# Kernel tuning notes

Hardware: AMD Instinct MI355X
Metric: run time of the kernel (lower is better)

Reference implementation:

```python
import jax, jax.numpy as jnp
import numpy as np

LN_EPS = 1e-5
NORM_EPS = 1e-12


def channel_layernorm(x, w, b):
    # LayerNorm over channel dim of NCHW tensor (torch permutes to NHWC; equivalent)
    mu = x.mean(axis=1, keepdims=True)
    var = x.var(axis=1, keepdims=True)
    xn = (x - mu) / jnp.sqrt(var + LN_EPS)
    return xn * w[None, :, None, None] + b[None, :, None, None]


def pconv(x, w):
    # 1x1 pointwise conv, w: (out_ch, in_ch)
    return jnp.einsum('bchw,oc->bohw', x, w)


def dwconv3(x, w):
    # depthwise 3x3, padding 1; w: (ch, 1, 3, 3)
    return jax.lax.conv_general_dilated(
        x, w, window_strides=(1, 1), padding='SAME',
        feature_group_count=x.shape[1],
        dimension_numbers=('NCHW', 'OIHW', 'NCHW'))


def l2norm(x):
    n = jnp.sqrt(jnp.sum(x * x, axis=-1, keepdims=True))
    return x / jnp.maximum(n, NORM_EPS)


def setup_inputs() -> dict:
    key = jax.random.key(0)
    ks = jax.random.split(key, 8)
    B, C, H, W = 4, 128, 128, 128
    NH, G = 8, 2

    def w(k, shape, fan_in):
        return jax.random.normal(k, shape, dtype=jnp.float32) * (fan_in ** -0.5)

    return {
        'x': jax.random.normal(ks[0], (B, C, H, W), dtype=jnp.float32),
        'ln1_w': jnp.ones((C,), jnp.float32),
        'ln1_b': jnp.zeros((C,), jnp.float32),
        'temperature': jnp.ones((NH, 1, 1), jnp.float32),
        'qkv_p_w': w(ks[1], (3 * C, C), C),
        'qkv_d_w': w(ks[2], (3 * C, 1, 3, 3), 9),
        'proj_w': w(ks[3], (C, C), C),
        'ln2_w': jnp.ones((C,), jnp.float32),
        'ln2_b': jnp.zeros((C,), jnp.float32),
        'g1_w': w(ks[4], (2 * G * C, C), C),
        'gd_w': w(ks[5], (2 * G * C, 1, 3, 3), 9),
        'g2_w': w(ks[6], (C, G * C), G * C),
        'num_heads': NH,
    }


def reference(x, ln1_w, ln1_b, temperature, qkv_p_w, qkv_d_w, proj_w,
              ln2_w, ln2_b, g1_w, gd_w, g2_w, num_heads):
    b, c, h, w_ = x.shape
    d = c // num_heads

    # --- MDTA branch ---
    y = channel_layernorm(x, ln1_w, ln1_b)
    qkv = dwconv3(pconv(y, qkv_p_w), qkv_d_w)  # (b, 3c, h, w)
    q, k, v = jnp.split(qkv, 3, axis=1)
    q = l2norm(q.reshape(b, num_heads, d, h * w_))
    k = l2norm(k.reshape(b, num_heads, d, h * w_))
    v = v.reshape(b, num_heads, d, h * w_)
    # transposed (channel) attention: (b, heads, d, d)
    attn = jnp.einsum('bhdn,bhen->bhde', q, k) * temperature[None]
    attn = jax.nn.softmax(attn, axis=-1)
    out = jnp.einsum('bhde,bhen->bhdn', attn, v).reshape(b, c, h, w_)
    x = x + pconv(out, proj_w)

    # --- GDFN branch ---
    y = channel_layernorm(x, ln2_w, ln2_b)
    hdn = dwconv3(pconv(y, g1_w), gd_w)  # (b, 2*gamma*c, h, w)
    x1, x2 = jnp.split(hdn, 2, axis=1)
    g = jax.nn.gelu(x1, approximate=False) * x2
    x = x + pconv(g, g2_w)
    return x
```

## Files before the change

### kernel.cpp

```cpp
#include <hip/hip_runtime.h>
#include <cstdint>
#include <cstddef>

typedef float f32x4 __attribute__((ext_vector_type(4)));
typedef __bf16 bf16x8 __attribute__((ext_vector_type(8)));

__device__ __forceinline__ float b2f(unsigned short u) {
    union { unsigned int i; float f; } z; z.i = ((unsigned int)u) << 16; return z.f;
}
__device__ __forceinline__ unsigned short f2b(float f) {
    union { float f; unsigned int i; } z; z.f = f;
    unsigned int x = z.i;
    return (unsigned short)((x + 0x7FFFu + ((x >> 16) & 1u)) >> 16);
}

static constexpr int C = 128;
static constexpr int NP = 16384;
static constexpr int NH = 8;

struct Ptr11 { const float* p[11]; };
__constant__ int kWN[11]   = {128, 128, 8, 49152, 3456, 16384, 128, 128, 65536, 4608, 32768};
__constant__ int kWOff[11] = {0, 128, 256, 272, 49424, 52880, 69264, 69392, 69520, 135056, 139664};
static constexpr int kWTotal = 172432;

__global__ __launch_bounds__(256)
void cvt_w_kernel(Ptr11 P, unsigned short* __restrict__ dst)
{
    int seg = blockIdx.y;
    int n = kWN[seg];
    int i = blockIdx.x * 256 + threadIdx.x;
    if (i >= n) return;
    dst[kWOff[seg] + i] = f2b(P.p[seg][i]);
}

template <int COUT>
__device__ __forceinline__ void gemm_core_128(
    const unsigned short (*Bs)[128],
    const unsigned short* __restrict__ W,
    unsigned short* __restrict__ OutB,
    int n0, int tid)
{
    const int lane = tid & 63;
    const int wid  = tid >> 6;
    const int ln16 = lane & 15, quad = lane >> 4;
    const int wy = wid >> 1, wx = wid & 1;
    for (int cc = 0; cc < COUT / 128; ++cc) {
        const int m0 = cc * 128;
        f32x4 acc[4][4];
        #pragma unroll
        for (int i = 0; i < 4; ++i)
            #pragma unroll
            for (int j = 0; j < 4; ++j) acc[i][j] = f32x4{0.f, 0.f, 0.f, 0.f};

        #pragma unroll
        for (int k0 = 0; k0 < 128; k0 += 32) {
            bf16x8 afr[4], bfr[4];
            #pragma unroll
            for (int mt = 0; mt < 4; ++mt) {
                int m = m0 + wy * 64 + mt * 16 + ln16;
                uint4 v = *(const uint4*)(W + (size_t)m * 128 + k0 + quad * 8);
                afr[mt] = *(bf16x8*)&v;
            }
            #pragma unroll
            for (int nt = 0; nt < 4; ++nt) {
                int n = wx * 64 + nt * 16 + ln16;
                union { bf16x8 v; unsigned short u[8]; } tmp;
                #pragma unroll
                for (int j = 0; j < 8; ++j) tmp.u[j] = Bs[k0 + quad * 8 + j][n];
                bfr[nt] = tmp.v;
            }
            #pragma unroll
            for (int mt = 0; mt < 4; ++mt)
                #pragma unroll
                for (int nt = 0; nt < 4; ++nt)
                    acc[mt][nt] = __builtin_amdgcn_mfma_f32_16x16x32_bf16(
                        afr[mt], bfr[nt], acc[mt][nt], 0, 0, 0);
        }
        #pragma unroll
        for (int mt = 0; mt < 4; ++mt)
            #pragma unroll
            for (int nt = 0; nt < 4; ++nt) {
                int co0 = m0 + wy * 64 + mt * 16 + quad * 4;
                int n = n0 + wx * 64 + nt * 16 + ln16;
                #pragma unroll
                for (int r = 0; r < 4; ++r)
                    OutB[(size_t)(co0 + r) * NP + n] = f2b(acc[mt][nt][r]);
            }
    }
}

template <int COUT>
__global__ __launch_bounds__(256)
void lngemm_kernel(const float* __restrict__ x,
                   const unsigned short* __restrict__ lg,
                   const unsigned short* __restrict__ lb,
                   const unsigned short* __restrict__ W,
                   unsigned short* __restrict__ Out)
{
    __shared__ unsigned short Bs[128][128];
    __shared__ float Ssum[8][128], Ssq[8][128], Mu[128], Rs[128];
    const int tid = threadIdx.x;
    const int b = blockIdx.y;
    const int n0 = blockIdx.x * 128;
    const int pxg = tid & 31;
    const int cseg = tid >> 5;
    const float* xb = x + (size_t)b * C * NP + n0 + pxg * 4;

    f32x4 hv[16];
    f32x4 vs = f32x4{0.f, 0.f, 0.f, 0.f}, vq = f32x4{0.f, 0.f, 0.f, 0.f};
    #pragma unroll
    for (int i = 0; i < 16; ++i) {
        f32x4 v = *(const f32x4*)(xb + (size_t)(cseg * 16 + i) * NP);
        hv[i] = v; vs += v; vq += v * v;
    }
    #pragma unroll
    for (int j = 0; j < 4; ++j) {
        Ssum[cseg][pxg * 4 + j] = vs[j];
        Ssq[cseg][pxg * 4 + j]  = vq[j];
    }
    __syncthreads();
    if (tid < 128) {
        float s = 0.f, q = 0.f;
        #pragma unroll
        for (int e = 0; e < 8; ++e) { s += Ssum[e][tid]; q += Ssq[e][tid]; }
        float mu = s * (1.f / 128.f);
        float var = q * (1.f / 128.f) - mu * mu;
        Mu[tid] = mu;
        Rs[tid] = rsqrtf(fmaxf(var, 0.f) + 1e-5f);
    }
    __syncthreads();
    f32x4 mu4 = *(const f32x4*)(&Mu[pxg * 4]);
    f32x4 rs4 = *(const f32x4*)(&Rs[pxg * 4]);
    #pragma unroll
    for (int i = 0; i < 16; ++i) {
        int c = cseg * 16 + i;
        float gw = b2f(lg[c]), bw = b2f(lb[c]);
        union { uint2 v; unsigned short u[4]; } o;
        #pragma unroll
        for (int j = 0; j < 4; ++j)
            o.u[j] = f2b((hv[i][j] - mu4[j]) * rs4[j] * gw + bw);
        *(uint2*)(&Bs[c][pxg * 4]) = o.v;
    }
    __syncthreads();
    gemm_core_128<COUT>(Bs, W, Out + (size_t)b * COUT * NP, n0, tid);
}

template <int COUT>
__global__ __launch_bounds__(256)
void gemm_bf16_kernel(const unsigned short* __restrict__ W,
                      const unsigned short* __restrict__ X,
                      unsigned short* __restrict__ Out)
{
    __shared__ unsigned short Bs[128][128];
    const int tid = threadIdx.x;
    const int b = blockIdx.y;
    const int n0 = blockIdx.x * 128;
    const unsigned short* Xb = X + (size_t)b * 128 * NP;
    #pragma unroll
    for (int r = 0; r < 8; ++r) {
        int flat = tid + r * 256;
        int kk = flat >> 4, nn = (flat & 15) * 8;
        *(uint4*)(&Bs[kk][nn]) = *(const uint4*)(Xb + (size_t)kk * NP + n0 + nn);
    }
    __syncthreads();
    gemm_core_128<COUT>(Bs, W, Out + (size_t)b * COUT * NP, n0, tid);
}

__global__ __launch_bounds__(256)
void projln_kernel(const unsigned short* __restrict__ W,
                   const unsigned short* __restrict__ Xin,
                   const float* __restrict__ Res,
                   float* __restrict__ Xmid,
                   const unsigned short* __restrict__ lg,
                   const unsigned short* __restrict__ lb,
                   unsigned short* __restrict__ Y2)
{
    __shared__ unsigned short Bs[128][128];
    __shared__ float RedS[2][128], RedQ[2][128], Mu[128], Rs[128];
    const int tid = threadIdx.x;
    const int b = blockIdx.y;
    const int n0 = blockIdx.x * 128;
    const unsigned short* Xb = Xin + (size_t)b * 128 * NP;
    #pragma unroll
    for (int r = 0; r < 8; ++r) {
        int flat = tid + r * 256;
        int kk = flat >> 4, nn = (flat & 15) * 8;
        *(uint4*)(&Bs[kk][nn]) = *(const uint4*)(Xb + (size_t)kk * NP + n0 + nn);
    }
    __syncthreads();

    const int lane = tid & 63, wid = tid >> 6;
    const int ln16 = lane & 15, quad = lane >> 4;
    const int wy = wid >> 1, wx = wid & 1;

    f32x4 acc[4][4];
    #pragma unroll
    for (int i = 0; i < 4; ++i)
        #pragma unroll
        for (int j = 0; j < 4; ++j) acc[i][j] = f32x4{0.f, 0.f, 0.f, 0.f};

    #pragma unroll
    for (int k0 = 0; k0 < 128; k0 += 32) {
        bf16x8 afr[4], bfr[4];
        #pragma unroll
        for (int mt = 0; mt < 4; ++mt) {
            int m = wy * 64 + mt * 16 + ln16;
            uint4 v = *(const uint4*)(W + (size_t)m * 128 + k0 + quad * 8);
            afr[mt] = *(bf16x8*)&v;
        }
        #pragma unroll
        for (int nt = 0; nt < 4; ++nt) {
            int n = wx * 64 + nt * 16 + ln16;
            union { bf16x8 v; unsigned short u[8]; } tmp;
            #pragma unroll
            for (int j = 0; j < 8; ++j) tmp.u[j] = Bs[k0 + quad * 8 + j][n];
            bfr[nt] = tmp.v;
        }
        #pragma unroll
        for (int mt = 0; mt < 4; ++mt)
            #pragma unroll
            for (int nt = 0; nt < 4; ++nt)
                acc[mt][nt] = __builtin_amdgcn_mfma_f32_16x16x32_bf16(
                    afr[mt], bfr[nt], acc[mt][nt], 0, 0, 0);
    }

    size_t base = (size_t)b * 128 * NP;
    float ps[4] = {0.f, 0.f, 0.f, 0.f}, pq[4] = {0.f, 0.f, 0.f, 0.f};
    #pragma unroll
    for (int mt = 0; mt < 4; ++mt)
        #pragma unroll
        for (int nt = 0; nt < 4; ++nt) {
            int co0 = wy * 64 + mt * 16 + quad * 4;
            int n = n0 + wx * 64 + nt * 16 + ln16;
            #pragma unroll
            for (int r = 0; r < 4; ++r) {
                size_t idx = base + (size_t)(co0 + r) * NP + n;
                float t = Res[idx] + acc[mt][nt][r];
                Xmid[idx] = t;
                acc[mt][nt][r] = t;
                ps[nt] += t; pq[nt] += t * t;
            }
        }
    #pragma unroll
    for (int nt = 0; nt < 4; ++nt) {
        ps[nt] += __shfl_xor(ps[nt], 16, 64); ps[nt] += __shfl_xor(ps[nt], 32, 64);
        pq[nt] += __shfl_xor(pq[nt], 16, 64); pq[nt] += __shfl_xor(pq[nt], 32, 64);
    }
    if (quad == 0) {
        #pragma unroll
        for (int nt = 0; nt < 4; ++nt) {
            int nn = wx * 64 + nt * 16 + ln16;
            RedS[wy][nn] = ps[nt]; RedQ[wy][nn] = pq[nt];
        }
    }
    __syncthreads();
    if (tid < 128) {
        float s = RedS[0][tid] + RedS[1][tid];
        float q = RedQ[0][tid] + RedQ[1][tid];
        float mu = s * (1.f / 128.f);
        float var = q * (1.f / 128.f) - mu * mu;
        Mu[tid] = mu; Rs[tid] = rsqrtf(fmaxf(var, 0.f) + 1e-5f);
    }
    __syncthreads();

    #pragma unroll
    for (int mt = 0; mt < 4; ++mt) {
        int co0 = wy * 64 + mt * 16 + quad * 4;
        union { uint2 v; unsigned short u[4]; } gv, bv;
        gv.v = *(const uint2*)(lg + co0);
        bv.v = *(const uint2*)(lb + co0);
        float gw[4], bw[4];
        #pragma unroll
        for (int r = 0; r < 4; ++r) { gw[r] = b2f(gv.u[r]); bw[r] = b2f(bv.u[r]); }
        #pragma unroll
        for (int nt = 0; nt < 4; ++nt) {
            int nn = wx * 64 + nt * 16 + ln16;
            float mu = Mu[nn], rs = Rs[nn];
            int n = n0 + nn;
            #pragma unroll
            for (int r = 0; r < 4; ++r) {
                size_t idx = base + (size_t)(co0 + r) * NP + n;
                Y2[idx] = f2b((acc[mt][nt][r] - mu) * rs * gw[r] + bw[r]);
            }
        }
    }
}

template <int K, int EPI>
__global__ __launch_bounds__(256)
void gemm_pconv(const unsigned short* __restrict__ W,
                const unsigned short* __restrict__ X,
                void* __restrict__ Out,
                const float* __restrict__ Res,
                int Cout)
{
    __shared__ unsigned short Bs[32][128];
    const int tid = threadIdx.x;
    const int b = blockIdx.z;
    const int n0 = blockIdx.x * 128;
    const int m0 = blockIdx.y * 128;
    const unsigned short* Xb = X + (size_t)b * K * NP;
    const int wid = tid >> 6;
    const int lane = tid & 63;
    const int ln16 = lane & 15;
    const int quad = lane >> 4;
    const int wy = wid >> 1;
    const int wx = wid & 1;

    f32x4 acc[4][4];
    #pragma unroll
    for (int i = 0; i < 4; ++i)
        #pragma unroll
        for (int j = 0; j < 4; ++j)
            acc[i][j] = f32x4{0.f, 0.f, 0.f, 0.f};

    for (int k0 = 0; k0 < K; k0 += 32) {
        #pragma unroll
        for (int r = 0; r < 2; ++r) {
            int flat = tid + r * 256;
            int kk = flat >> 4;
            int nn = (flat & 15) * 8;
            uint4 v = *(const uint4*)(Xb + (size_t)(k0 + kk) * NP + n0 + nn);
            *(uint4*)(&Bs[kk][nn]) = v;
        }
        __syncthreads();

        bf16x8 afr[4];
        #pragma unroll
        for (int mt = 0; mt < 4; ++mt) {
            int m = m0 + wy * 64 + mt * 16 + ln16;
            uint4 v = *(const uint4*)(W + (size_t)m * K + k0 + quad * 8);
            afr[mt] = *(bf16x8*)&v;
        }
        bf16x8 bfr[4];
        #pragma unroll
        for (int nt = 0; nt < 4; ++nt) {
            int n = wx * 64 + nt * 16 + ln16;
            union { bf16x8 v; unsigned short u[8]; } tmp;
            #pragma unroll
            for (int j = 0; j < 8; ++j) tmp.u[j] = Bs[quad * 8 + j][n];
            bfr[nt] = tmp.v;
        }
        #pragma unroll
        for (int mt = 0; mt < 4; ++mt)
            #pragma unroll
            for (int nt = 0; nt < 4; ++nt)
                acc[mt][nt] = __builtin_amdgcn_mfma_f32_16x16x32_bf16(
                    afr[mt], bfr[nt], acc[mt][nt], 0, 0, 0);
        __syncthreads();
    }

    size_t outbase = (size_t)b * Cout * NP;
    #pragma unroll
    for (int mt = 0; mt < 4; ++mt) {
        #pragma unroll
        for (int nt = 0; nt < 4; ++nt) {
            int co0 = m0 + wy * 64 + mt * 16 + quad * 4;
            int n = n0 + wx * 64 + nt * 16 + ln16;
            #pragma unroll
            for (int r = 0; r < 4; ++r) {
                float v = acc[mt][nt][r];
                size_t idx = outbase + (size_t)(co0 + r) * NP + n;
                if (EPI == 0) ((unsigned short*)Out)[idx] = f2b(v);
                else          ((float*)Out)[idx] = Res[idx] + v;
            }
        }
    }
}

__global__ __launch_bounds__(256)
void dwconv3_kernel(const unsigned short* __restrict__ in,
                    const unsigned short* __restrict__ w9,
                    unsigned short* __restrict__ out, int CH)
{
    int t = blockIdx.x * 256 + threadIdx.x;
    int xi = (t & 15) * 8;
    int y  = (t >> 4) & 127;
    int bc = t >> 11;
    int c  = bc % CH;
    const unsigned short* base = in + (size_t)bc * NP + y * 128 + xi;

    float wr[9];
    #pragma unroll
    for (int i = 0; i < 9; ++i) wr[i] = b2f(w9[c * 9 + i]);

    uint4 rv0 = uint4{0,0,0,0}, rv1, rv2 = uint4{0,0,0,0};
    if (y > 0)   rv0 = *(const uint4*)(base - 128);
    rv1 = *(const uint4*)(base);
    if (y < 127) rv2 = *(const uint4*)(base + 128);
    uint4 rows[3] = {rv0, rv1, rv2};

    float o[8];
    #pragma unroll
    for (int j = 0; j < 8; ++j) o[j] = 0.f;

    #pragma unroll
    for (int r = 0; r < 3; ++r) {
        union { uint4 v; unsigned short u[8]; } cv; cv.v = rows[r];
        int lh = __shfl_up((int)cv.u[7], 1, 16);
        int rh = __shfl_down((int)cv.u[0], 1, 16);
        float p[10];
        p[0] = (xi > 0)   ? b2f((unsigned short)lh) : 0.f;
        p[9] = (xi < 120) ? b2f((unsigned short)rh) : 0.f;
        #pragma unroll
        for (int j = 0; j < 8; ++j) p[j + 1] = b2f(cv.u[j]);
        #pragma unroll
        for (int j = 0; j < 8; ++j)
            o[j] += wr[r * 3] * p[j] + wr[r * 3 + 1] * p[j + 1] + wr[r * 3 + 2] * p[j + 2];
    }
    union { uint4 v; unsigned short u[8]; } res;
    #pragma unroll
    for (int j = 0; j < 8; ++j) res.u[j] = f2b(o[j]);
    *(uint4*)(out + (size_t)bc * NP + y * 128 + xi) = res.v;
}

__global__ __launch_bounds__(256)
void dwgelu_kernel(const unsigned short* __restrict__ hdn,
                   const unsigned short* __restrict__ w9,
                   unsigned short* __restrict__ g)
{
    int t = blockIdx.x * 256 + threadIdx.x;
    int xi = (t & 15) * 8;
    int y  = (t >> 4) & 127;
    int bc = t >> 11;
    int c  = bc & 255;
    int b  = bc >> 8;
    const unsigned short* base1 = hdn + ((size_t)b * 512 + c) * NP + y * 128 + xi;
    const unsigned short* base2 = base1 + (size_t)256 * NP;

    float w1[9], w2[9];
    #pragma unroll
    for (int i = 0; i < 9; ++i) {
        w1[i] = b2f(w9[c * 9 + i]);
        w2[i] = b2f(w9[(c + 256) * 9 + i]);
    }

    uint4 ra0 = uint4{0,0,0,0}, ra1, ra2 = uint4{0,0,0,0};
    uint4 rb0 = uint4{0,0,0,0}, rb1, rb2 = uint4{0,0,0,0};
    if (y > 0)   { ra0 = *(const uint4*)(base1 - 128); rb0 = *(const uint4*)(base2 - 128); }
    ra1 = *(const uint4*)(base1);
    rb1 = *(const uint4*)(base2);
    if (y < 127) { ra2 = *(const uint4*)(base1 + 128); rb2 = *(const uint4*)(base2 + 128); }
    uint4 rowsA[3] = {ra0, ra1, ra2};
    uint4 rowsB[3] = {rb0, rb1, rb2};

    float a1[8], a2[8];
    #pragma unroll
    for (int j = 0; j < 8; ++j) { a1[j] = 0.f; a2[j] = 0.f; }

    #pragma unroll
    for (int r = 0; r < 3; ++r) {
        union { uint4 v; unsigned short u[8]; } c1, c2;
        c1.v = rowsA[r]; c2.v = rowsB[r];
        int lh1 = __shfl_up((int)c1.u[7], 1, 16);
        int rh1 = __shfl_down((int)c1.u[0], 1, 16);
        int lh2 = __shfl_up((int)c2.u[7], 1, 16);
        int rh2 = __shfl_down((int)c2.u[0], 1, 16);
        float p1[10], p2[10];
        p1[0] = (xi > 0)   ? b2f((unsigned short)lh1) : 0.f;
        p1[9] = (xi < 120) ? b2f((unsigned short)rh1) : 0.f;
        p2[0] = (xi > 0)   ? b2f((unsigned short)lh2) : 0.f;
        p2[9] = (xi < 120) ? b2f((unsigned short)rh2) : 0.f;
        #pragma unroll
        for (int j = 0; j < 8; ++j) { p1[j + 1] = b2f(c1.u[j]); p2[j + 1] = b2f(c2.u[j]); }
        #pragma unroll
        for (int j = 0; j < 8; ++j) {
            a1[j] += w1[r * 3] * p1[j] + w1[r * 3 + 1] * p1[j + 1] + w1[r * 3 + 2] * p1[j + 2];
            a2[j] += w2[r * 3] * p2[j] + w2[r * 3 + 1] * p2[j + 1] + w2[r * 3 + 2] * p2[j + 2];
        }
    }
    union { uint4 v; unsigned short u[8]; } res;
    #pragma unroll
    for (int j = 0; j < 8; ++j) {
        float u = a1[j];
        float tt = u * (0.7978845608f + 0.0356774081f * u * u);
        float e = __expf(2.f * tt);
        float th = 1.f - 2.f / (e + 1.f);
        float ge = 0.5f * u * (1.f + th);
        res.u[j] = f2b(ge * a2[j]);
    }
    *(uint4*)(g + (size_t)bc * NP + y * 128 + xi) = res.v;
}

__global__ __launch_bounds__(256)
void gramss_kernel(const unsigned short* __restrict__ qkv,
                   float* __restrict__ Spart, float* __restrict__ Npart)
{
    int h = blockIdx.x, b = blockIdx.y, sp = blockIdx.z;
    int wid = threadIdx.x >> 6, lane = threadIdx.x & 63;
    int ln16 = lane & 15, quad = lane >> 4;
    int nbase = sp * 2048 + wid * 512;
    const unsigned short* qp = qkv + ((size_t)b * 384 + h * 16 + ln16) * NP;
    const unsigned short* kp = qkv + ((size_t)b * 384 + 128 + h * 16 + ln16) * NP;
    f32x4 acc = f32x4{0.f, 0.f, 0.f, 0.f};
    float qs = 0.f, ks = 0.f;
    for (int i = 0; i < 512; i += 32) {
        int n = nbase + i + quad * 8;
        uint4 av = *(const uint4*)(qp + n);
        uint4 bv = *(const uint4*)(kp + n);
        union { uint4 v; unsigned short u[8]; } ua, ub;
        ua.v = av; ub.v = bv;
        #pragma unroll
        for (int j = 0; j < 8; ++j) {
            float qv = b2f(ua.u[j]); qs += qv * qv;
            float kv = b2f(ub.u[j]); ks += kv * kv;
        }
        acc = __builtin_amdgcn_mfma_f32_16x16x32_bf16(*(bf16x8*)&av, *(bf16x8*)&bv, acc, 0, 0, 0);
    }
    int bh = b * NH + h;
    float* Sp = Spart + ((size_t)bh * 32 + sp * 4 + wid) * 256;
    #pragma unroll
    for (int r = 0; r < 4; ++r)
        Sp[(quad * 4 + r) * 16 + ln16] = acc[r];

    qs += __shfl_xor(qs, 16, 64); qs += __shfl_xor(qs, 32, 64);
    ks += __shfl_xor(ks, 16, 64); ks += __shfl_xor(ks, 32, 64);
    __shared__ float G[4][32];
    if (quad == 0) { G[wid][ln16] = qs; G[wid][16 + ln16] = ks; }
    __syncthreads();
    if (threadIdx.x < 32) {
        float s = G[0][threadIdx.x] + G[1][threadIdx.x] + G[2][threadIdx.x] + G[3][threadIdx.x];
        Npart[((size_t)bh * 8 + sp) * 32 + threadIdx.x] = s;
    }
}

__global__ __launch_bounds__(256)
void softmax2_kernel(const float* __restrict__ Spart, const float* __restrict__ Npart,
                     const unsigned short* __restrict__ temp, float* __restrict__ P)
{
    int bh = blockIdx.x;
    int h = bh & 7;
    int t = threadIdx.x;
    int dq = t >> 4, dk = t & 15;
    float sacc = 0.f;
    const float* Sp = Spart + (size_t)bh * 32 * 256;
    #pragma unroll
    for (int j = 0; j < 32; ++j) sacc += Sp[j * 256 + t];
    const float* Np = Npart + (size_t)bh * 8 * 32;
    float sq = 0.f, sk = 0.f;
    #pragma unroll
    for (int sp = 0; sp < 8; ++sp) { sq += Np[sp * 32 + dq]; sk += Np[sp * 32 + 16 + dk]; }
    float nq = fmaxf(sqrtf(sq), 1e-12f);
    float nk = fmaxf(sqrtf(sk), 1e-12f);
    float v = sacc / (nq * nk) * b2f(temp[h]);
    float m = v;
    #pragma unroll
    for (int o = 8; o > 0; o >>= 1) m = fmaxf(m, __shfl_xor(m, o, 16));
    float e = __expf(v - m);
    float s = e;
    #pragma unroll
    for (int o = 8; o > 0; o >>= 1) s += __shfl_xor(s, o, 16);
    P[(size_t)bh * 256 + t] = e / s;
}

__global__ __launch_bounds__(256)
void attnv_kernel(const float* __restrict__ P, const unsigned short* __restrict__ qkv,
                  unsigned short* __restrict__ out)
{
    __shared__ float Ps[256];
    int h = blockIdx.y, b = blockIdx.z;
    Ps[threadIdx.x] = P[((size_t)b * NH + h) * 256 + threadIdx.x];
    __syncthreads();
    int n = (blockIdx.x * 256 + threadIdx.x) * 4;
    const unsigned short* vp = qkv + ((size_t)b * 384 + 256 + h * 16) * NP + n;
    float o[16][4];
    #pragma unroll
    for (int d = 0; d < 16; ++d)
        #pragma unroll
        for (int j = 0; j < 4; ++j) o[d][j] = 0.f;
    #pragma unroll
    for (int e = 0; e < 16; ++e) {
        union { uint2 v; unsigned short u[4]; } cv;
        cv.v = *(const uint2*)(vp + (size_t)e * NP);
        float v0 = b2f(cv.u[0]), v1 = b2f(cv.u[1]), v2 = b2f(cv.u[2]), v3 = b2f(cv.u[3]);
        #pragma unroll
        for (int d = 0; d < 16; ++d) {
            float p = Ps[d * 16 + e];
            o[d][0] += p * v0; o[d][1] += p * v1; o[d][2] += p * v2; o[d][3] += p * v3;
        }
    }
    unsigned short* op = out + ((size_t)b * C + h * 16) * NP + n;
    #pragma unroll
    for (int d = 0; d < 16; ++d) {
        union { uint2 v; unsigned short u[4]; } res;
        #pragma unroll
        for (int j = 0; j < 4; ++j) res.u[j] = f2b(o[d][j]);
        *(uint2*)(op + (size_t)d * NP) = res.v;
    }
}

struct Bufs {
    float* xmid;
    unsigned short* y;
    unsigned short* y2;
    unsigned short* big;
    unsigned short* mid;
    float* Spart;
    float* P;
    float* Npart;
};

static void run_pipeline(const float* x_f32, float* out_f32,
                         const unsigned short* w,
                         const Bufs& B, int nb, hipStream_t stream)
{
    const unsigned short* ln1_w   = w + 0;
    const unsigned short* ln1_b   = w + 128;
    const unsigned short* temp    = w + 256;
    const unsigned short* qkv_p_w = w + 272;
    const unsigned short* qkv_d_w = w + 49424;
    const unsigned short* proj_w  = w + 52880;
    const unsigned short* ln2_w   = w + 69264;
    const unsigned short* ln2_b   = w + 69392;
    const unsigned short* g1_w    = w + 69520;
    const unsigned short* gd_w    = w + 135056;
    const unsigned short* g2_w    = w + 139664;

    lngemm_kernel<384><<<dim3(NP / 128, nb), 256, 0, stream>>>(x_f32, ln1_w, ln1_b, qkv_p_w, B.big);
    dwconv3_kernel<<<nb * 384 * NP / 2048, 256, 0, stream>>>(B.big, qkv_d_w, B.mid, 384);
    gramss_kernel<<<dim3(NH, nb, 8), 256, 0, stream>>>(B.mid, B.Spart, B.Npart);
    softmax2_kernel<<<nb * NH, 256, 0, stream>>>(B.Spart, B.Npart, temp, B.P);
    attnv_kernel<<<dim3(NP / 1024, NH, nb), 256, 0, stream>>>(B.P, B.mid, B.y);
    projln_kernel<<<dim3(NP / 128, nb), 256, 0, stream>>>(proj_w, B.y, x_f32, B.xmid, ln2_w, ln2_b, B.y2);

    gemm_bf16_kernel<512><<<dim3(NP / 128, nb), 256, 0, stream>>>(g1_w, B.y2, B.big);
    dwgelu_kernel<<<nb * 256 * NP / 2048, 256, 0, stream>>>(B.big, gd_w, B.mid);
    gemm_pconv<256, 1><<<dim3(NP / 128, 1, nb), 256, 0, stream>>>(g2_w, B.mid, out_f32, B.xmid, 128);
}

extern "C" void kernel_launch(void* const* d_in, const int* in_sizes, int n_in,
                              void* d_out, int out_size, void* d_ws, size_t ws_size,
                              hipStream_t stream)
{
    (void)in_sizes; (void)n_in; (void)out_size;
    const float* x = (const float*)d_in[0];
    char* ws = (char*)d_ws;

    size_t off = 0;
    unsigned short* wpack = (unsigned short*)(ws + off);
    off += (size_t)kWTotal * 2;
    off = (off + 255) & ~(size_t)255;
    size_t header = off;

    auto layout = [&](int nb, size_t o, Bufs& B) -> size_t {
        B.xmid = (float*)(ws + o);           o += (size_t)nb * C * NP * 4;
        B.y    = (unsigned short*)(ws + o);  o += (size_t)nb * C * NP * 2;
        B.y2   = (unsigned short*)(ws + o);  o += (size_t)nb * C * NP * 2;
        B.big  = (unsigned short*)(ws + o);  o += (size_t)nb * 512 * NP * 2;
        B.mid  = (unsigned short*)(ws + o);  o += (size_t)nb * 384 * NP * 2;
        B.Spart = (float*)(ws + o);          o += (size_t)nb * NH * 32 * 256 * 4;
        B.P     = (float*)(ws + o);          o += (size_t)nb * NH * 256 * 4;
        B.Npart = (float*)(ws + o);          o += (size_t)nb * NH * 8 * 32 * 4;
        return o;
    };

    Ptr11 P;
    for (int i = 0; i < 11; ++i) P.p[i] = (const float*)d_in[i + 1];
    cvt_w_kernel<<<dim3(256, 11), 256, 0, stream>>>(P, wpack);

    Bufs Bfull;
    size_t need_full = layout(4, header, Bfull);

    if (ws_size >= need_full) {
        run_pipeline(x, (float*)d_out, wpack, Bfull, 4, stream);
    } else {
        Bufs B1;
        layout(1, header, B1);
        for (int b = 0; b < 4; ++b) {
            run_pipeline(x + (size_t)b * C * NP,
                         (float*)d_out + (size_t)b * C * NP,
                         wpack, B1, 1, stream);
        }
    }
}
```

Measured before the change: 265.9 us.

## Store GEMM B operands pixel-major with XOR-swizzled LDS for vector fragment loads

Intermediate activations y and y2 move from channel-major to pixel-major layout, so the GEMM B tiles can be staged in LDS transposed and XOR-swizzled. Each MFMA B fragment then comes from one 16-byte LDS read instead of eight strided 2-byte reads, which removes LDS bank conflicts and instruction overhead. attnv and projln now write the transposed layout, and projln does it through an LDS round-trip so its global stores stay coalesced. gemm_pconv pads its LDS rows to 130 to reduce bank conflicts, at the cost of scalar 32-bit stores into LDS.

```diff
diff --git a/kernel.cpp b/kernel.cpp
--- a/kernel.cpp
+++ b/kernel.cpp
@@ -34,8 +34,8 @@
 }
 
 template <int COUT>
-__device__ __forceinline__ void gemm_core_128(
-    const unsigned short (*Bs)[128],
+__device__ __forceinline__ void gemm_core_tr(
+    const unsigned short* BsT,
     const unsigned short* __restrict__ W,
     unsigned short* __restrict__ OutB,
     int n0, int tid)
@@ -44,6 +44,15 @@
     const int wid  = tid >> 6;
     const int ln16 = lane & 15, quad = lane >> 4;
     const int wy = wid >> 1, wx = wid & 1;
+    const char* bs = (const char*)BsT;
+    const int swz = (ln16 & 7) << 4;
+    int rbase[4];
+    #pragma unroll
+    for (int nt = 0; nt < 4; ++nt) {
+        int n = wx * 64 + nt * 16 + ln16;
+        rbase[nt] = n * 256 + quad * 16;
+    }
+
     for (int cc = 0; cc < COUT / 128; ++cc) {
         const int m0 = cc * 128;
         f32x4 acc[4][4];
@@ -63,11 +72,8 @@
             }
             #pragma unroll
             for (int nt = 0; nt < 4; ++nt) {
-                int n = wx * 64 + nt * 16 + ln16;
-                union { bf16x8 v; unsigned short u[8]; } tmp;
-                #pragma unroll
-                for (int j = 0; j < 8; ++j) tmp.u[j] = Bs[k0 + quad * 8 + j][n];
-                bfr[nt] = tmp.v;
+                uint4 v = *(const uint4*)(bs + ((rbase[nt] + k0 * 2) ^ swz));
+                bfr[nt] = *(bf16x8*)&v;
             }
             #pragma unroll
             for (int mt = 0; mt < 4; ++mt)
@@ -97,7 +103,7 @@
                    const unsigned short* __restrict__ W,
                    unsigned short* __restrict__ Out)
 {
-    __shared__ unsigned short Bs[128][128];
+    __shared__ unsigned short BsT[128 * 128];
     __shared__ float Ssum[8][128], Ssq[8][128], Mu[128], Rs[128];
     const int tid = threadIdx.x;
     const int b = blockIdx.y;
@@ -131,67 +137,91 @@
     __syncthreads();
     f32x4 mu4 = *(const f32x4*)(&Mu[pxg * 4]);
     f32x4 rs4 = *(const f32x4*)(&Rs[pxg * 4]);
+
+    float gwv[16], bwv[16];
     #pragma unroll
     for (int i = 0; i < 16; ++i) {
-        int c = cseg * 16 + i;
-        float gw = b2f(lg[c]), bw = b2f(lb[c]);
-        union { uint2 v; unsigned short u[4]; } o;
-        #pragma unroll
-        for (int j = 0; j < 4; ++j)
-            o.u[j] = f2b((hv[i][j] - mu4[j]) * rs4[j] * gw + bw);
-        *(uint2*)(&Bs[c][pxg * 4]) = o.v;
-    }
-    __syncthreads();
-    gemm_core_128<COUT>(Bs, W, Out + (size_t)b * COUT * NP, n0, tid);
+        gwv[i] = b2f(lg[cseg * 16 + i]);
+        bwv[i] = b2f(lb[cseg * 16 + i]);
+    }
+
+    char* p = (char*)BsT;
+    #pragma unroll
+    for (int j = 0; j < 4; ++j) {
+        int n = pxg * 4 + j;
+        union { uint4 v[2]; unsigned short u[16]; } o;
+        #pragma unroll
+        for (int i = 0; i < 16; ++i)
+            o.u[i] = f2b((hv[i][j] - mu4[j]) * rs4[j] * gwv[i] + bwv[i]);
+        int base = n * 256 + cseg * 32;
+        int sw = (n & 7) << 4;
+        *(uint4*)(p + (base ^ sw))        = o.v[0];
+        *(uint4*)(p + ((base + 16) ^ sw)) = o.v[1];
+    }
+    __syncthreads();
+    gemm_core_tr<COUT>(BsT, W, Out + (size_t)b * COUT * NP, n0, tid);
 }
 
 template <int COUT>
 __global__ __launch_bounds__(256)
-void gemm_bf16_kernel(const unsigned short* __restrict__ W,
-                      const unsigned short* __restrict__ X,
-                      unsigned short* __restrict__ Out)
-{
-    __shared__ unsigned short Bs[128][128];
+void gemm_bf16t_kernel(const unsigned short* __restrict__ W,
+                       const unsigned short* __restrict__ Xt,
+                       unsigned short* __restrict__ Out)
+{
+    __shared__ unsigned short BsT[128 * 128];
     const int tid = threadIdx.x;
     const int b = blockIdx.y;
     const int n0 = blockIdx.x * 128;
-    const unsigned short* Xb = X + (size_t)b * 128 * NP;
+    const unsigned short* Xb = Xt + (size_t)b * NP * 128 + (size_t)n0 * 128;
+    char* p = (char*)BsT;
     #pragma unroll
     for (int r = 0; r < 8; ++r) {
         int flat = tid + r * 256;
-        int kk = flat >> 4, nn = (flat & 15) * 8;
-        *(uint4*)(&Bs[kk][nn]) = *(const uint4*)(Xb + (size_t)kk * NP + n0 + nn);
-    }
-    __syncthreads();
-    gemm_core_128<COUT>(Bs, W, Out + (size_t)b * COUT * NP, n0, tid);
+        int n = flat >> 4, ks = flat & 15;
+        uint4 v = *(const uint4*)(Xb + (size_t)n * 128 + ks * 8);
+        *(uint4*)(p + ((n * 256 + ks * 16) ^ ((n & 7) << 4))) = v;
+    }
+    __syncthreads();
+    gemm_core_tr<COUT>(BsT, W, Out + (size_t)b * COUT * NP, n0, tid);
 }
 
 __global__ __launch_bounds__(256)
 void projln_kernel(const unsigned short* __restrict__ W,
-                   const unsigned short* __restrict__ Xin,
+                   const unsigned short* __restrict__ Yt,
                    const float* __restrict__ Res,
                    float* __restrict__ Xmid,
                    const unsigned short* __restrict__ lg,
                    const unsigned short* __restrict__ lb,
-                   unsigned short* __restrict__ Y2)
-{
-    __shared__ unsigned short Bs[128][128];
+                   unsigned short* __restrict__ Y2t)
+{
+    __shared__ unsigned short BsT[128 * 128];
     __shared__ float RedS[2][128], RedQ[2][128], Mu[128], Rs[128];
     const int tid = threadIdx.x;
     const int b = blockIdx.y;
     const int n0 = blockIdx.x * 128;
-    const unsigned short* Xb = Xin + (size_t)b * 128 * NP;
-    #pragma unroll
-    for (int r = 0; r < 8; ++r) {
-        int flat = tid + r * 256;
-        int kk = flat >> 4, nn = (flat & 15) * 8;
-        *(uint4*)(&Bs[kk][nn]) = *(const uint4*)(Xb + (size_t)kk * NP + n0 + nn);
+    char* p = (char*)BsT;
+    {
+        const unsigned short* Xb = Yt + (size_t)b * NP * 128 + (size_t)n0 * 128;
+        #pragma unroll
+        for (int r = 0; r < 8; ++r) {
+            int flat = tid + r * 256;
+            int n = flat >> 4, ks = flat & 15;
+            uint4 v = *(const uint4*)(Xb + (size_t)n * 128 + ks * 8);
+            *(uint4*)(p + ((n * 256 + ks * 16) ^ ((n & 7) << 4))) = v;
+        }
     }
     __syncthreads();
 
     const int lane = tid & 63, wid = tid >> 6;
     const int ln16 = lane & 15, quad = lane >> 4;
     const int wy = wid >> 1, wx = wid & 1;
+    const int swz = (ln16 & 7) << 4;
+    int rbase[4];
+    #pragma unroll
+    for (int nt = 0; nt < 4; ++nt) {
+        int n = wx * 64 + nt * 16 + ln16;
+        rbase[nt] = n * 256 + quad * 16;
+    }
 
     f32x4 acc[4][4];
     #pragma unroll
@@ -210,11 +240,8 @@
         }
         #pragma unroll
         for (int nt = 0; nt < 4; ++nt) {
-            int n = wx * 64 + nt * 16 + ln16;
-            union { bf16x8 v; unsigned short u[8]; } tmp;
-            #pragma unroll
-            for (int j = 0; j < 8; ++j) tmp.u[j] = Bs[k0 + quad * 8 + j][n];
-            bfr[nt] = tmp.v;
+            uint4 v = *(const uint4*)(p + ((rbase[nt] + k0 * 2) ^ swz));
+            bfr[nt] = *(bf16x8*)&v;
         }
         #pragma unroll
         for (int mt = 0; mt < 4; ++mt)
@@ -276,13 +303,23 @@
         for (int nt = 0; nt < 4; ++nt) {
             int nn = wx * 64 + nt * 16 + ln16;
             float mu = Mu[nn], rs = Rs[nn];
-            int n = n0 + nn;
-            #pragma unroll
-            for (int r = 0; r < 4; ++r) {
-                size_t idx = base + (size_t)(co0 + r) * NP + n;
-                Y2[idx] = f2b((acc[mt][nt][r] - mu) * rs * gw[r] + bw[r]);
-            }
-        }
+            union { uint2 v; unsigned short u[4]; } t2;
+            #pragma unroll
+            for (int r = 0; r < 4; ++r)
+                t2.u[r] = f2b((acc[mt][nt][r] - mu) * rs * gw[r] + bw[r]);
+            int addr = (nn * 256 + co0 * 2) ^ ((nn & 7) << 4);
+            *(uint2*)(p + addr) = t2.v;
+        }
+    }
+    __syncthreads();
+
+    unsigned short* Yo = Y2t + (size_t)b * NP * 128 + (size_t)n0 * 128;
+    #pragma unroll
+    for (int r = 0; r < 8; ++r) {
+        int flat = tid + r * 256;
+        int n = flat >> 4, ks = flat & 15;
+        uint4 v = *(const uint4*)(p + ((n * 256 + ks * 16) ^ ((n & 7) << 4)));
+        *(uint4*)(Yo + (size_t)n * 128 + ks * 8) = v;
     }
 }
 
@@ -294,7 +331,7 @@
                 const float* __restrict__ Res,
                 int Cout)
 {
-    __shared__ unsigned short Bs[32][128];
+    __shared__ unsigned short Bs[32][130];
     const int tid = threadIdx.x;
     const int b = blockIdx.z;
     const int n0 = blockIdx.x * 128;
@@ -321,7 +358,8 @@
             int kk = flat >> 4;
             int nn = (flat & 15) * 8;
             uint4 v = *(const uint4*)(Xb + (size_t)(k0 + kk) * NP + n0 + nn);
-            *(uint4*)(&Bs[kk][nn]) = v;
+            unsigned int* d = (unsigned int*)&Bs[kk][nn];
+            d[0] = v.x; d[1] = v.y; d[2] = v.z; d[3] = v.w;
         }
         __syncthreads();
 
@@ -555,7 +593,7 @@
 
 __global__ __launch_bounds__(256)
 void attnv_kernel(const float* __restrict__ P, const unsigned short* __restrict__ qkv,
-                  unsigned short* __restrict__ out)
+                  unsigned short* __restrict__ yt)
 {
     __shared__ float Ps[256];
     int h = blockIdx.y, b = blockIdx.z;
@@ -579,13 +617,16 @@
             o[d][0] += p * v0; o[d][1] += p * v1; o[d][2] += p * v2; o[d][3] += p * v3;
         }
     }
-    unsigned short* op = out + ((size_t)b * C + h * 16) * NP + n;
-    #pragma unroll
-    for (int d = 0; d < 16; ++d) {
-        union { uint2 v; unsigned short u[4]; } res;
-        #pragma unroll
-        for (int j = 0; j < 4; ++j) res.u[j] = f2b(o[d][j]);
-        *(uint2*)(op + (size_t)d * NP) = res.v;
+    unsigned short* op = yt + (size_t)b * NP * C + (size_t)n * C + h * 16;
+    #pragma unroll
+    for (int j = 0; j < 4; ++j) {
+        union { uint4 v; unsigned short u[8]; } r1, r2;
+        #pragma unroll
+        for (int d = 0; d < 8; ++d) r1.u[d] = f2b(o[d][j]);
+        #pragma unroll
+        for (int d = 0; d < 8; ++d) r2.u[d] = f2b(o[8 + d][j]);
+        *(uint4*)(op + (size_t)j * C)     = r1.v;
+        *(uint4*)(op + (size_t)j * C + 8) = r2.v;
     }
 }
 
@@ -623,7 +664,7 @@
     attnv_kernel<<<dim3(NP / 1024, NH, nb), 256, 0, stream>>>(B.P, B.mid, B.y);
     projln_kernel<<<dim3(NP / 128, nb), 256, 0, stream>>>(proj_w, B.y, x_f32, B.xmid, ln2_w, ln2_b, B.y2);
 
-    gemm_bf16_kernel<512><<<dim3(NP / 128, nb), 256, 0, stream>>>(g1_w, B.y2, B.big);
+    gemm_bf16t_kernel<512><<<dim3(NP / 128, nb), 256, 0, stream>>>(g1_w, B.y2, B.big);
     dwgelu_kernel<<<nb * 256 * NP / 2048, 256, 0, stream>>>(B.big, gd_w, B.mid);
     gemm_pconv<256, 1><<<dim3(NP / 128, 1, nb), 256, 0, stream>>>(g2_w, B.mid, out_f32, B.xmid, 128);
 }
```

Result: no change. 266.7 us (+0.3%).
